# Kernel optimization log

Measured on AMD Instinct MI355X. Metric: run time of the kernel, lower is better.

Reference implementation:

```python
import jax, jax.numpy as jnp
import numpy as np
from jax import lax

WINDOW_SIZE = 11
SIGMA = 1.5
C1 = 0.01 ** 2
C2 = 0.03 ** 2


def _gaussian_window(window_size, sigma, channel):
    # 1D gaussian, normalized, then outer product -> 2D window
    x = np.arange(window_size) - window_size // 2
    g = np.exp(-(x.astype(np.float64) ** 2) / (2.0 * sigma ** 2))
    g = (g / g.sum()).astype(np.float32)
    w2d = np.outer(g, g)  # [K, K]
    # depthwise kernel [C, 1, K, K] (OIHW with feature_group_count=C)
    w = np.broadcast_to(w2d, (channel, 1, window_size, window_size))
    return jnp.asarray(np.ascontiguousarray(w))


def _depthwise_conv(x, w, channel):
    pad = WINDOW_SIZE // 2
    return lax.conv_general_dilated(
        x, w,
        window_strides=(1, 1),
        padding=[(pad, pad), (pad, pad)],
        dimension_numbers=("NCHW", "OIHW", "NCHW"),
        feature_group_count=channel,
    )


def setup_inputs() -> dict:
    key = jax.random.key(0)
    k1, k2 = jax.random.split(key)
    B, C, H, W = 32, 3, 512, 512
    img1 = jax.random.uniform(k1, (B, C, H, W), dtype=jnp.float32)
    img2 = jax.random.uniform(k2, (B, C, H, W), dtype=jnp.float32)
    return {"img1": img1, "img2": img2}


def reference(img1, img2):
    channel = img1.shape[1]
    window = _gaussian_window(WINDOW_SIZE, SIGMA, channel)

    mu1 = _depthwise_conv(img1, window, channel)
    mu2 = _depthwise_conv(img2, window, channel)

    mu1_sq = mu1 * mu1
    mu2_sq = mu2 * mu2
    mu1_mu2 = mu1 * mu2

    sigma1_sq = _depthwise_conv(img1 * img1, window, channel) - mu1_sq
    sigma2_sq = _depthwise_conv(img2 * img2, window, channel) - mu2_sq
    sigma12 = _depthwise_conv(img1 * img2, window, channel) - mu1_mu2

    sigma1_sq = jnp.maximum(sigma1_sq, 0.0)
    sigma2_sq = jnp.maximum(sigma2_sq, 0.0)

    numerator = (2.0 * mu1_mu2 + C1) * (2.0 * sigma12 + C2)
    denominator = (mu1_sq + mu2_sq + C1) * (sigma1_sq + sigma2_sq + C2)
    ssim_map = jnp.clip(numerator / denominator, 0.0, 1.0)

    return 1.0 - jnp.mean(ssim_map)
```

## Files before the change

kernel.cpp:

```cpp
#include <hip/hip_runtime.h>


typedef float v2f __attribute__((ext_vector_type(2)));
typedef float v4f __attribute__((ext_vector_type(4)));

constexpr int IMG    = 512;
constexpr int TPB    = 256;
constexpr int SH     = 64;
constexpr int NPAIR  = 37;
constexpr int LW     = 272;
constexpr int PLANES = 32 * 3;
constexpr double N_PIX = 25165824.0;

__global__ __launch_bounds__(TPB, 3) void ssim_map_kernel(
    const float* __restrict__ img1, const float* __restrict__ img2,
    double* __restrict__ partial)
{
    constexpr float GW[11] = {
        0.0010283801f, 0.0075987583f, 0.0360007721f, 0.1093607008f,
        0.2130055439f, 0.2660117257f, 0.2130055439f, 0.1093607008f,
        0.0360007721f, 0.0075987583f, 0.0010283801f };
    constexpr float GWp[13] = {
        0.0f,
        0.0010283801f, 0.0075987583f, 0.0360007721f, 0.1093607008f,
        0.2130055439f, 0.2660117257f, 0.2130055439f, 0.1093607008f,
        0.0360007721f, 0.0075987583f, 0.0010283801f,
        0.0f };

    __shared__ v4f  sbuf[3][LW];
    __shared__ float wsum[TPB / 64];

    const int tid   = threadIdx.x;
    const int x0    = blockIdx.x * TPB;
    const int y0    = blockIdx.y * SH;
    const int plane = blockIdx.z;

    const float* p1 = img1 + (size_t)plane * IMG * IMG;
    const float* p2 = img2 + (size_t)plane * IMG * IMG;

    const int  c   = x0 + tid - 8;
    const bool cok = (unsigned)c < (unsigned)IMG;
    const int  c2  = x0 + 248 + tid;
    const bool c2ok = (unsigned)c2 < (unsigned)IMG;

    v2f rg1[6], rg2[6], rg11[6], rg22[6], rg12[6];

    v2f accv = {0.0f, 0.0f};

    float pa1, pb1, pa2, pb2, qa1, qb1, qa2, qb2;
    auto prefetch = [&](int i) {
        const int  rA  = y0 - 5 + 2 * i;
        const int  rB  = rA + 1;
        const bool aok = (unsigned)rA < (unsigned)IMG;
        const bool bok = (unsigned)rB < (unsigned)IMG;
        const size_t oA = (size_t)rA * IMG;
        const size_t oB = (size_t)rB * IMG;
        pa1 = (aok && cok) ? p1[oA + c] : 0.0f;
        pb1 = (bok && cok) ? p1[oB + c] : 0.0f;
        pa2 = (aok && cok) ? p2[oA + c] : 0.0f;
        pb2 = (bok && cok) ? p2[oB + c] : 0.0f;
        if (tid < 16) {
            qa1 = (aok && c2ok) ? p1[oA + c2] : 0.0f;
            qb1 = (bok && c2ok) ? p1[oB + c2] : 0.0f;
            qa2 = (aok && c2ok) ? p2[oA + c2] : 0.0f;
            qb2 = (bok && c2ok) ? p2[oB + c2] : 0.0f;
        }
    };

    prefetch(0);

    for (int ib = 0; ib < NPAIR; ib += 6) {
#pragma unroll
        for (int j = 0; j < 6; ++j) {
            const int i = ib + j;
            if (i < NPAIR) {
                sbuf[j % 3][tid] = v4f{pa1, pb1, pa2, pb2};
                if (tid < 16) sbuf[j % 3][256 + tid] = v4f{qa1, qb1, qa2, qb2};

                __syncthreads();

                if (i + 1 < NPAIR) prefetch(i + 1);

                v2f a1 = {0,0}, a2 = {0,0}, a11 = {0,0}, a22 = {0,0}, a12 = {0,0};
                const v4f* sp = &sbuf[j % 3][tid + 3];
#pragma unroll
                for (int k = 0; k < 11; ++k) {
                    const v4f s  = sp[k];
                    const v2f x1 = __builtin_shufflevector(s, s, 0, 1);
                    const v2f x2 = __builtin_shufflevector(s, s, 2, 3);
                    const float g = GW[k];
                    const v2f t1 = g * x1;
                    const v2f t2 = g * x2;
                    a1 += t1;
                    a2 += t2;
                    a11 = __builtin_elementwise_fma(t1, x1, a11);
                    a22 = __builtin_elementwise_fma(t2, x2, a22);
                    a12 = __builtin_elementwise_fma(t1, x2, a12);
                }
                rg1[j] = a1;  rg2[j] = a2;
                rg11[j] = a11; rg22[j] = a22; rg12[j] = a12;
            }

            if (i >= 5 && i < NPAIR) {
                v2f sx1={0,0}, sy1={0,0}, sx2={0,0}, sy2={0,0};
                v2f sx11={0,0}, sy11={0,0}, sx22={0,0}, sy22={0,0};
                v2f sx12={0,0}, sy12={0,0};
#pragma unroll
                for (int m = 0; m < 6; ++m) {
                    const int s = (j + 1 + m) % 6;
                    const v2f wx = { GWp[2*m + 1], GWp[2*m + 2] };
                    const v2f wy = { GWp[2*m],     GWp[2*m + 1] };
                    sx1  = __builtin_elementwise_fma(wx, rg1[s],  sx1);
                    sy1  = __builtin_elementwise_fma(wy, rg1[s],  sy1);
                    sx2  = __builtin_elementwise_fma(wx, rg2[s],  sx2);
                    sy2  = __builtin_elementwise_fma(wy, rg2[s],  sy2);
                    sx11 = __builtin_elementwise_fma(wx, rg11[s], sx11);
                    sy11 = __builtin_elementwise_fma(wy, rg11[s], sy11);
                    sx22 = __builtin_elementwise_fma(wx, rg22[s], sx22);
                    sy22 = __builtin_elementwise_fma(wy, rg22[s], sy22);
                    sx12 = __builtin_elementwise_fma(wx, rg12[s], sx12);
                    sy12 = __builtin_elementwise_fma(wy, rg12[s], sy12);
                }
                const v2f m1  = { sx1.x + sx1.y,  sy1.x + sy1.y };
                const v2f m2  = { sx2.x + sx2.y,  sy2.x + sy2.y };
                const v2f e11 = { sx11.x + sx11.y, sy11.x + sy11.y };
                const v2f e22 = { sx22.x + sx22.y, sy22.x + sy22.y };
                const v2f e12 = { sx12.x + sx12.y, sy12.x + sy12.y };

                const v2f mu11 = m1 * m1;
                const v2f mu22 = m2 * m2;
                const v2f mu12 = m1 * m2;
                const v2f zero = {0.0f, 0.0f};
                const v2f one  = {1.0f, 1.0f};
                const v2f sg1  = __builtin_elementwise_max(e11 - mu11, zero);
                const v2f sg2  = __builtin_elementwise_max(e22 - mu22, zero);
                const v2f sg12 = e12 - mu12;
                const v2f num = (2.0f * mu12 + 1e-4f) * (2.0f * sg12 + 9e-4f);
                const v2f den = (mu11 + mu22 + 1e-4f) * (sg1 + sg2 + 9e-4f);
                v2f v = { num.x * __builtin_amdgcn_rcpf(den.x),
                          num.y * __builtin_amdgcn_rcpf(den.y) };
                v = __builtin_elementwise_min(__builtin_elementwise_max(v, zero), one);
                accv += v;
            }
        }
    }

    float acc = accv.x + accv.y;
#pragma unroll
    for (int off = 32; off > 0; off >>= 1)
        acc += __shfl_down(acc, off, 64);
    if ((tid & 63) == 0) wsum[tid >> 6] = acc;
    __syncthreads();
    if (tid == 0) {
        double blocksum = 0.0;
#pragma unroll
        for (int w = 0; w < TPB / 64; ++w) blocksum += (double)wsum[w];
        atomicAdd(partial, blocksum);
    }
}

__global__ void ssim_finalize_kernel(const double* __restrict__ partial,
                                     float* __restrict__ out)
{
    out[0] = 1.0f - (float)(partial[0] / N_PIX);
}

extern "C" void kernel_launch(void* const* d_in, const int* in_sizes, int n_in,
                              void* d_out, int out_size, void* d_ws, size_t ws_size,
                              hipStream_t stream) {
    const float* img1 = (const float*)d_in[0];
    const float* img2 = (const float*)d_in[1];
    float* out = (float*)d_out;
    double* acc = (double*)d_ws;

    hipMemsetAsync(acc, 0, sizeof(double), stream);

    dim3 grid(IMG / TPB, IMG / SH, PLANES);
    ssim_map_kernel<<<grid, TPB, 0, stream>>>(img1, img2, acc);
    ssim_finalize_kernel<<<1, 1, 0, stream>>>(acc, out);
}
```

Before: 249.9 us.

## Process two row-pairs per barrier with two-deep global prefetch

```diff
diff --git a/kernel.cpp b/kernel.cpp
--- a/kernel.cpp
+++ b/kernel.cpp
@@ -27,7 +27,7 @@
         0.0360007721f, 0.0075987583f, 0.0010283801f,
         0.0f };
 
-    __shared__ v4f  sbuf[3][LW];
+    __shared__ v4f  sbuf[4][LW];
     __shared__ float wsum[TPB / 64];
 
     const int tid   = threadIdx.x;
@@ -48,7 +48,9 @@
     v2f accv = {0.0f, 0.0f};
 
     float pa1, pb1, pa2, pb2, qa1, qb1, qa2, qb2;
-    auto prefetch = [&](int i) {
+    float ra1, rb1, ra2, rb2, sa1, sb1, sa2, sb2;
+
+    auto prefetchA = [&](int i) {
         const int  rA  = y0 - 5 + 2 * i;
         const int  rB  = rA + 1;
         const bool aok = (unsigned)rA < (unsigned)IMG;
@@ -66,82 +68,118 @@
             qb2 = (bok && c2ok) ? p2[oB + c2] : 0.0f;
         }
     };
-
-    prefetch(0);
-
-    for (int ib = 0; ib < NPAIR; ib += 6) {
-#pragma unroll
-        for (int j = 0; j < 6; ++j) {
-            const int i = ib + j;
-            if (i < NPAIR) {
-                sbuf[j % 3][tid] = v4f{pa1, pb1, pa2, pb2};
-                if (tid < 16) sbuf[j % 3][256 + tid] = v4f{qa1, qb1, qa2, qb2};
-
-                __syncthreads();
-
-                if (i + 1 < NPAIR) prefetch(i + 1);
-
-                v2f a1 = {0,0}, a2 = {0,0}, a11 = {0,0}, a22 = {0,0}, a12 = {0,0};
-                const v4f* sp = &sbuf[j % 3][tid + 3];
-#pragma unroll
-                for (int k = 0; k < 11; ++k) {
-                    const v4f s  = sp[k];
-                    const v2f x1 = __builtin_shufflevector(s, s, 0, 1);
-                    const v2f x2 = __builtin_shufflevector(s, s, 2, 3);
-                    const float g = GW[k];
-                    const v2f t1 = g * x1;
-                    const v2f t2 = g * x2;
-                    a1 += t1;
-                    a2 += t2;
-                    a11 = __builtin_elementwise_fma(t1, x1, a11);
-                    a22 = __builtin_elementwise_fma(t2, x2, a22);
-                    a12 = __builtin_elementwise_fma(t1, x2, a12);
-                }
-                rg1[j] = a1;  rg2[j] = a2;
-                rg11[j] = a11; rg22[j] = a22; rg12[j] = a12;
+    auto prefetchB = [&](int i) {
+        const int  rA  = y0 - 5 + 2 * i;
+        const int  rB  = rA + 1;
+        const bool aok = (unsigned)rA < (unsigned)IMG;
+        const bool bok = (unsigned)rB < (unsigned)IMG;
+        const size_t oA = (size_t)rA * IMG;
+        const size_t oB = (size_t)rB * IMG;
+        ra1 = (aok && cok) ? p1[oA + c] : 0.0f;
+        rb1 = (bok && cok) ? p1[oB + c] : 0.0f;
+        ra2 = (aok && cok) ? p2[oA + c] : 0.0f;
+        rb2 = (bok && cok) ? p2[oB + c] : 0.0f;
+        if (tid < 16) {
+            sa1 = (aok && c2ok) ? p1[oA + c2] : 0.0f;
+            sb1 = (bok && c2ok) ? p1[oB + c2] : 0.0f;
+            sa2 = (aok && c2ok) ? p2[oA + c2] : 0.0f;
+            sb2 = (bok && c2ok) ? p2[oB + c2] : 0.0f;
+        }
+    };
+
+    auto hconv = [&](int slot, int rs) {
+        v2f a1 = {0,0}, a2 = {0,0}, a11 = {0,0}, a22 = {0,0}, a12 = {0,0};
+        const v4f* sp = &sbuf[slot][tid + 3];
+#pragma unroll
+        for (int k = 0; k < 11; ++k) {
+            const v4f s  = sp[k];
+            const v2f x1 = __builtin_shufflevector(s, s, 0, 1);
+            const v2f x2 = __builtin_shufflevector(s, s, 2, 3);
+            const float g = GW[k];
+            const v2f t1 = g * x1;
+            const v2f t2 = g * x2;
+            a1 += t1;
+            a2 += t2;
+            a11 = __builtin_elementwise_fma(t1, x1, a11);
+            a22 = __builtin_elementwise_fma(t2, x2, a22);
+            a12 = __builtin_elementwise_fma(t1, x2, a12);
+        }
+        rg1[rs] = a1;  rg2[rs] = a2;
+        rg11[rs] = a11; rg22[rs] = a22; rg12[rs] = a12;
+    };
+
+    auto vert = [&](int r) {
+        v2f sx1={0,0}, sy1={0,0}, sx2={0,0}, sy2={0,0};
+        v2f sx11={0,0}, sy11={0,0}, sx22={0,0}, sy22={0,0};
+        v2f sx12={0,0}, sy12={0,0};
+#pragma unroll
+        for (int m = 0; m < 6; ++m) {
+            const int s = (r + 1 + m) % 6;
+            const v2f wx = { GWp[2*m + 1], GWp[2*m + 2] };
+            const v2f wy = { GWp[2*m],     GWp[2*m + 1] };
+            sx1  = __builtin_elementwise_fma(wx, rg1[s],  sx1);
+            sy1  = __builtin_elementwise_fma(wy, rg1[s],  sy1);
+            sx2  = __builtin_elementwise_fma(wx, rg2[s],  sx2);
+            sy2  = __builtin_elementwise_fma(wy, rg2[s],  sy2);
+            sx11 = __builtin_elementwise_fma(wx, rg11[s], sx11);
+            sy11 = __builtin_elementwise_fma(wy, rg11[s], sy11);
+            sx22 = __builtin_elementwise_fma(wx, rg22[s], sx22);
+            sy22 = __builtin_elementwise_fma(wy, rg22[s], sy22);
+            sx12 = __builtin_elementwise_fma(wx, rg12[s], sx12);
+            sy12 = __builtin_elementwise_fma(wy, rg12[s], sy12);
+        }
+        const v2f m1  = { sx1.x + sx1.y,  sy1.x + sy1.y };
+        const v2f m2  = { sx2.x + sx2.y,  sy2.x + sy2.y };
+        const v2f e11 = { sx11.x + sx11.y, sy11.x + sy11.y };
+        const v2f e22 = { sx22.x + sx22.y, sy22.x + sy22.y };
+        const v2f e12 = { sx12.x + sx12.y, sy12.x + sy12.y };
+
+        const v2f mu11 = m1 * m1;
+        const v2f mu22 = m2 * m2;
+        const v2f mu12 = m1 * m2;
+        const v2f zero = {0.0f, 0.0f};
+        const v2f one  = {1.0f, 1.0f};
+        const v2f sg1  = __builtin_elementwise_max(e11 - mu11, zero);
+        const v2f sg2  = __builtin_elementwise_max(e22 - mu22, zero);
+        const v2f sg12 = e12 - mu12;
+        const v2f num = (2.0f * mu12 + 1e-4f) * (2.0f * sg12 + 9e-4f);
+        const v2f den = (mu11 + mu22 + 1e-4f) * (sg1 + sg2 + 9e-4f);
+        v2f v = { num.x * __builtin_amdgcn_rcpf(den.x),
+                  num.y * __builtin_amdgcn_rcpf(den.y) };
+        v = __builtin_elementwise_min(__builtin_elementwise_max(v, zero), one);
+        accv += v;
+    };
+
+    prefetchA(0);
+    prefetchB(1);
+
+    for (int ib = 0; ib < NPAIR; ib += 12) {
+#pragma unroll
+        for (int jj = 0; jj < 6; ++jj) {
+            const int p0 = ib + 2 * jj;
+            const int p1i = p0 + 1;
+            const int s0 = (2 * jj) % 4;
+            const int s1 = (2 * jj + 1) % 4;
+            const int r0 = (2 * jj) % 6;
+            const int r1 = (2 * jj + 1) % 6;
+
+            if (p0 < NPAIR) {
+                sbuf[s0][tid] = v4f{pa1, pb1, pa2, pb2};
+                if (tid < 16) sbuf[s0][256 + tid] = v4f{qa1, qb1, qa2, qb2};
             }
-
-            if (i >= 5 && i < NPAIR) {
-                v2f sx1={0,0}, sy1={0,0}, sx2={0,0}, sy2={0,0};
-                v2f sx11={0,0}, sy11={0,0}, sx22={0,0}, sy22={0,0};
-                v2f sx12={0,0}, sy12={0,0};
-#pragma unroll
-                for (int m = 0; m < 6; ++m) {
-                    const int s = (j + 1 + m) % 6;
-                    const v2f wx = { GWp[2*m + 1], GWp[2*m + 2] };
-                    const v2f wy = { GWp[2*m],     GWp[2*m + 1] };
-                    sx1  = __builtin_elementwise_fma(wx, rg1[s],  sx1);
-                    sy1  = __builtin_elementwise_fma(wy, rg1[s],  sy1);
-                    sx2  = __builtin_elementwise_fma(wx, rg2[s],  sx2);
-                    sy2  = __builtin_elementwise_fma(wy, rg2[s],  sy2);
-                    sx11 = __builtin_elementwise_fma(wx, rg11[s], sx11);
-                    sy11 = __builtin_elementwise_fma(wy, rg11[s], sy11);
-                    sx22 = __builtin_elementwise_fma(wx, rg22[s], sx22);
-                    sy22 = __builtin_elementwise_fma(wy, rg22[s], sy22);
-                    sx12 = __builtin_elementwise_fma(wx, rg12[s], sx12);
-                    sy12 = __builtin_elementwise_fma(wy, rg12[s], sy12);
-                }
-                const v2f m1  = { sx1.x + sx1.y,  sy1.x + sy1.y };
-                const v2f m2  = { sx2.x + sx2.y,  sy2.x + sy2.y };
-                const v2f e11 = { sx11.x + sx11.y, sy11.x + sy11.y };
-                const v2f e22 = { sx22.x + sx22.y, sy22.x + sy22.y };
-                const v2f e12 = { sx12.x + sx12.y, sy12.x + sy12.y };
-
-                const v2f mu11 = m1 * m1;
-                const v2f mu22 = m2 * m2;
-                const v2f mu12 = m1 * m2;
-                const v2f zero = {0.0f, 0.0f};
-                const v2f one  = {1.0f, 1.0f};
-                const v2f sg1  = __builtin_elementwise_max(e11 - mu11, zero);
-                const v2f sg2  = __builtin_elementwise_max(e22 - mu22, zero);
-                const v2f sg12 = e12 - mu12;
-                const v2f num = (2.0f * mu12 + 1e-4f) * (2.0f * sg12 + 9e-4f);
-                const v2f den = (mu11 + mu22 + 1e-4f) * (sg1 + sg2 + 9e-4f);
-                v2f v = { num.x * __builtin_amdgcn_rcpf(den.x),
-                          num.y * __builtin_amdgcn_rcpf(den.y) };
-                v = __builtin_elementwise_min(__builtin_elementwise_max(v, zero), one);
-                accv += v;
+            if (p1i < NPAIR) {
+                sbuf[s1][tid] = v4f{ra1, rb1, ra2, rb2};
+                if (tid < 16) sbuf[s1][256 + tid] = v4f{sa1, sb1, sa2, sb2};
             }
+            if (p0 < NPAIR) __syncthreads();
+
+            if (p0 + 2 < NPAIR) prefetchA(p0 + 2);
+            if (p1i + 2 < NPAIR) prefetchB(p1i + 2);
+
+            if (p0 < NPAIR)              hconv(s0, r0);
+            if (p0 >= 5 && p0 < NPAIR)   vert(r0);
+            if (p1i < NPAIR)             hconv(s1, r1);
+            if (p1i >= 5 && p1i < NPAIR) vert(r1);
         }
     }
 
```

Result: slower. 256.8 us (+2.7%).
